# Kernel tuning notes

Measured on AMD Instinct MI355X. Metric: run time of the kernel, lower is better.

Reference implementation:

```python
import jax, jax.numpy as jnp
import numpy as np

S = 9                      # spiral length
V = [8192, 4096, 2048, 1024, 512]  # verts per level, finest -> latent


def grid_sample_bilinear(feat, grid):
    # feat [B,C,H,W], grid [B,P,2] in [-1,1]; bilinear, align_corners=True
    B, C, H, W = feat.shape
    x = (grid[..., 0] + 1.0) * 0.5 * (W - 1)
    y = (grid[..., 1] + 1.0) * 0.5 * (H - 1)
    x0 = jnp.floor(x); y0 = jnp.floor(y)
    wx = x - x0; wy = y - y0
    x0i = jnp.clip(x0.astype(jnp.int32), 0, W - 1)
    x1i = jnp.clip(x0.astype(jnp.int32) + 1, 0, W - 1)
    y0i = jnp.clip(y0.astype(jnp.int32), 0, H - 1)
    y1i = jnp.clip(y0.astype(jnp.int32) + 1, 0, H - 1)
    featf = feat.reshape(B, C, H * W).transpose(0, 2, 1)  # [B,HW,C]
    def gat(yi, xi):
        return jnp.take_along_axis(featf, (yi * W + xi)[..., None], axis=1)  # [B,P,C]
    w00 = ((1 - wy) * (1 - wx))[..., None]
    w01 = ((1 - wy) * wx)[..., None]
    w10 = (wy * (1 - wx))[..., None]
    w11 = (wy * wx)[..., None]
    return gat(y0i, x0i) * w00 + gat(y0i, x1i) * w01 + gat(y1i, x0i) * w10 + gat(y1i, x1i) * w11


def pool(x, row, col, val):
    # sparse mesh upsample: gather cols, scale, scatter-add into rows
    n_out = row.shape[0] // 3
    g = x[:, col, :] * val[None, :, None]                       # [B,nnz,C]
    return jnp.zeros((x.shape[0], n_out, x.shape[-1]), x.dtype).at[:, row, :].add(g)


def dsconv(x, idx, wd, wp, b):
    # depthwise-separable spiral conv: gather spiral ring, depthwise over S, pointwise mix
    g = x[:, idx]                                # [B,N,S,C]
    dw = jnp.einsum('bnsc,sc->bnc', g, wd)       # depthwise over spiral dim
    return jnp.einsum('bnc,co->bno', dw, wp) + b # pointwise


def _forward(uv, feat, upsample, s0, s1, s2, s3,
             row0, col0, val0, row1, col1, val1, row2, col2, val2, row3, col3, val3,
             wd0, wp0, b0, wd1, wp1, b1, wd2, wp2, b2, wd3, wp3, b3, wdh, wph, bh):
    uvc = jnp.clip((uv - 0.5) * 2.0, -1.0, 1.0)
    x = grid_sample_bilinear(feat, uvc)           # [B,P,C]  (torch: [B,C,P] then permute)
    x = jnp.einsum('vp,bpc->bvc', upsample, x)    # [B,V4,C] latent mesh features
    x = jax.nn.relu(dsconv(pool(x, row3, col3, val3), s3, wd0, wp0, b0))  # [B,1024,512]
    x = jax.nn.relu(dsconv(pool(x, row2, col2, val2), s2, wd1, wp1, b1))  # [B,2048,256]
    x = jax.nn.relu(dsconv(pool(x, row1, col1, val1), s1, wd2, wp2, b2))  # [B,4096,128]
    x = jax.nn.relu(dsconv(pool(x, row0, col0, val0), s0, wd3, wp3, b3))  # [B,8192,64]
    return dsconv(x, s0, wdh, wph, bh)            # [B,8192,3]


def setup_inputs():
    ks = jax.random.split(jax.random.key(0), 64)
    B, P, C, H, W = 8, 21, 512, 32, 32
    inp = {}
    inp['uv'] = jax.random.uniform(ks[0], (B, P, 2), jnp.float32)
    inp['feat'] = jax.random.normal(ks[1], (B, C, H, W), jnp.float32)
    inp['upsample'] = 0.01 * jnp.ones((V[4], P), jnp.float32)
    for i in range(4):
        inp[f's{i}'] = jax.random.randint(ks[2 + i], (V[i], S), 0, V[i])
    for i in range(4):
        nnz = 3 * V[i]
        inp[f'row{i}'] = jax.random.randint(ks[6 + 3 * i], (nnz,), 0, V[i])
        inp[f'col{i}'] = jax.random.randint(ks[7 + 3 * i], (nnz,), 0, V[i + 1])
        inp[f'val{i}'] = jax.random.uniform(ks[8 + 3 * i], (nnz,), jnp.float32)
    chans = [(512, 512), (512, 256), (256, 128), (128, 64), (64, 3)]
    names = ['0', '1', '2', '3', 'h']
    k = 20
    for (ci, co), nm in zip(chans, names):
        inp[f'wd{nm}'] = 0.1 * jax.random.normal(ks[k], (S, ci), jnp.float32); k += 1
        inp[f'wp{nm}'] = jax.random.normal(ks[k], (ci, co), jnp.float32) * (1.0 / float(np.sqrt(ci))); k += 1
        inp[f'b{nm}'] = jnp.zeros((co,), jnp.float32); k += 1
    return inp


def reference(uv, feat, upsample, s0, s1, s2, s3,
              row0, col0, val0, row1, col1, val1, row2, col2, val2, row3, col3, val3,
              wd0, wp0, b0, wd1, wp1, b1, wd2, wp2, b2, wd3, wp3, b3, wdh, wph, bh):
    return _forward(uv, feat, upsample, s0, s1, s2, s3,
                    row0, col0, val0, row1, col1, val1, row2, col2, val2, row3, col3, val3,
                    wd0, wp0, b0, wd1, wp1, b1, wd2, wp2, b2, wd3, wp3, b3, wdh, wph, bh)
```

## Files before the change

### kernel.cpp

```cpp
#include <hip/hip_runtime.h>

#define B_  8
#define P_  21
#define H_  32
#define W_  32

typedef float f32x4 __attribute__((ext_vector_type(4)));
typedef _Float16 f16x8 __attribute__((ext_vector_type(8)));

__device__ __forceinline__ void gload_lds16(const _Float16* g, _Float16* l) {
  __builtin_amdgcn_global_load_lds(
      (const __attribute__((address_space(1))) void*)g,
      (__attribute__((address_space(3))) void*)l, 16, 0, 0);
}

struct CsrParams {
  const int*   row[4];
  const int*   col[4];
  const float* val[4];
  int*   cnt[4];
  int*   rowptr[4];
  int*   colsout[4];
  float* valsout[4];
  int    nnz[4];
  int    V[4];
};

struct BsplitParams {
  const float* wp[4];
  int K[4], N[4], off[4];
  _Float16* b0;
  _Float16* b1;
};

__global__ __launch_bounds__(256) void k1_zero_sample(
    int* zp, int zn,
    const float* __restrict__ uv,
    const float* __restrict__ feat,
    float* __restrict__ xs) {
  int bid = blockIdx.x;
  if (bid < 60) {
    int i = bid * 256 + threadIdx.x;
    if (i < zn) zp[i] = 0;
    return;
  }
  int bp = bid - 60;
  int b  = bp / P_;
  float u0 = uv[bp * 2 + 0], u1 = uv[bp * 2 + 1];
  float gx = fminf(fmaxf((u0 - 0.5f) * 2.0f, -1.0f), 1.0f);
  float gy = fminf(fmaxf((u1 - 0.5f) * 2.0f, -1.0f), 1.0f);
  float fx = (gx + 1.0f) * 0.5f * (W_ - 1);
  float fy = (gy + 1.0f) * 0.5f * (H_ - 1);
  float x0f = floorf(fx), y0f = floorf(fy);
  float wx = fx - x0f, wy = fy - y0f;
  int x0 = (int)x0f, y0 = (int)y0f;
  int x0i = min(max(x0, 0), W_ - 1), x1i = min(max(x0 + 1, 0), W_ - 1);
  int y0i = min(max(y0, 0), H_ - 1), y1i = min(max(y0 + 1, 0), H_ - 1);
  float w00 = (1.f - wy) * (1.f - wx), w01 = (1.f - wy) * wx;
  float w10 = wy * (1.f - wx),        w11 = wy * wx;
  for (int c = threadIdx.x; c < 512; c += blockDim.x) {
    const float* fb = feat + ((size_t)(b * 512 + c)) * (H_ * W_);
    float v = fb[y0i * W_ + x0i] * w00 + fb[y0i * W_ + x1i] * w01 +
              fb[y1i * W_ + x0i] * w10 + fb[y1i * W_ + x1i] * w11;
    xs[(size_t)bp * 512 + c] = v;
  }
}

__global__ __launch_bounds__(256) void k2_count_upsample(
    CsrParams p,
    const float* __restrict__ up,
    const float* __restrict__ xs,
    float* __restrict__ xu) {
  int bid = blockIdx.x;
  if (bid < 384) {
    int l = bid / 96;
    int k = (bid - l * 96) * 256 + threadIdx.x;
    if (k < p.nnz[l]) atomicAdd(&p.cnt[l][p.row[l][k]], 1);
    return;
  }
  int b2 = bid - 384;
  int b = b2 >> 9, v = b2 & 511;
  int c2 = threadIdx.x << 1;
  float2 acc = make_float2(0.f, 0.f);
  for (int q = 0; q < P_; ++q) {
    float u = up[v * P_ + q];
    const float2 xv = *(const float2*)&xs[((size_t)(b * P_ + q)) * 512 + c2];
    acc.x = fmaf(u, xv.x, acc.x);
    acc.y = fmaf(u, xv.y, acc.y);
  }
  *(float2*)&xu[((size_t)(b * 512 + v)) * 512 + c2] = acc;
}

__global__ __launch_bounds__(256) void k3_scan_bsplit(CsrParams p, BsplitParams bp) {
  int bid = blockIdx.x;
  if (bid < 4) {
    int l = bid;
    int V = p.V[l];
    int* cnt = p.cnt[l];
    int* rp  = p.rowptr[l];
    int t = threadIdx.x;
    int chunk = V / 256;
    int base = t * chunk;
    int s = 0;
    for (int i = 0; i < chunk; ++i) s += cnt[base + i];
    __shared__ int sm[256];
    sm[t] = s;
    __syncthreads();
    for (int off = 1; off < 256; off <<= 1) {
      int v = (t >= off) ? sm[t - off] : 0;
      __syncthreads();
      sm[t] += v;
      __syncthreads();
    }
    int run = sm[t] - s;
    for (int i = 0; i < chunk; ++i) {
      int c = cnt[base + i];
      rp[base + i]  = run;
      cnt[base + i] = run;
      run += c;
    }
    if (t == 255) rp[V] = run;
    return;
  }
  int idx = (bid - 4) * 256 + threadIdx.x;
  #pragma unroll
  for (int t = 0; t < 4; ++t) {
    int sz = bp.N[t] * bp.K[t];
    if (idx < sz) {
      int K = bp.K[t];
      int n = idx / K, k = idx - n * K;
      float v = bp.wp[t][(size_t)k * bp.N[t] + n];
      _Float16 h0 = (_Float16)v;
      float r = (v - (float)h0) * 2048.0f;
      int ks = ((((k >> 3) ^ (n & 7)) << 3) | (k & 7));
      bp.b0[bp.off[t] + (size_t)n * K + ks] = h0;
      bp.b1[bp.off[t] + (size_t)n * K + ks] = (_Float16)r;
      return;
    }
    idx -= sz;
  }
}

__global__ void fill_kernel(CsrParams p) {
  int l = blockIdx.y;
  int k = blockIdx.x * 256 + threadIdx.x;
  if (k < p.nnz[l]) {
    int r = p.row[l][k];
    int pos = atomicAdd(&p.cnt[l][r], 1);
    p.colsout[l][pos] = p.col[l][k];
    p.valsout[l][pos] = p.val[l][k];
  }
}

__global__ __launch_bounds__(256) void pool_kernel(
    const float* __restrict__ x,
    const int* __restrict__ rowptr,
    const int* __restrict__ cols,
    const float* __restrict__ vals,
    float* __restrict__ out,
    int Vout, int Vin, int Cin) {
  const int lpr    = Cin >> 3;
  const int lshift = 31 - __clz(lpr);
  const int rpb    = 256 >> lshift;
  const int lr = threadIdx.x >> lshift;
  const int lc = threadIdx.x & (lpr - 1);
  const int b  = blockIdx.x & 7;
  const int n  = (blockIdx.x >> 3) * rpb + lr;
  const int c8 = lc << 3;
  const float* xb = x + (size_t)b * Vin * Cin + c8;
  int j0 = rowptr[n], j1 = rowptr[n + 1];
  int cnt = j1 - j0;
  float4 a0 = make_float4(0.f, 0.f, 0.f, 0.f);
  float4 a1 = make_float4(0.f, 0.f, 0.f, 0.f);
  if (cnt > 0) {
    int   cc[4];
    float vv[4];
    #pragma unroll
    for (int k = 0; k < 4; ++k) {
      int jj = j0 + ((k < cnt) ? k : 0);
      cc[k] = cols[jj];
      vv[k] = (k < cnt) ? vals[jj] : 0.f;
    }
    #pragma unroll
    for (int k = 0; k < 4; ++k) {
      const float* xr = xb + (size_t)cc[k] * Cin;
      float4 x0 = *(const float4*)xr;
      float4 x1 = *(const float4*)(xr + 4);
      float v = vv[k];
      a0.x = fmaf(v, x0.x, a0.x); a0.y = fmaf(v, x0.y, a0.y);
      a0.z = fmaf(v, x0.z, a0.z); a0.w = fmaf(v, x0.w, a0.w);
      a1.x = fmaf(v, x1.x, a1.x); a1.y = fmaf(v, x1.y, a1.y);
      a1.z = fmaf(v, x1.z, a1.z); a1.w = fmaf(v, x1.w, a1.w);
    }
    for (int j = j0 + 4; j < j1; ++j) {
      float v = vals[j];
      const float* xr = xb + (size_t)cols[j] * Cin;
      float4 x0 = *(const float4*)xr;
      float4 x1 = *(const float4*)(xr + 4);
      a0.x = fmaf(v, x0.x, a0.x); a0.y = fmaf(v, x0.y, a0.y);
      a0.z = fmaf(v, x0.z, a0.z); a0.w = fmaf(v, x0.w, a0.w);
      a1.x = fmaf(v, x1.x, a1.x); a1.y = fmaf(v, x1.y, a1.y);
      a1.z = fmaf(v, x1.z, a1.z); a1.w = fmaf(v, x1.w, a1.w);
    }
  }
  float* op = &out[((size_t)b * Vout + n) * Cin + c8];
  *(float4*)op = a0;
  *(float4*)(op + 4) = a1;
}

__global__ __launch_bounds__(256) void dw_split_kernel(
    const float* __restrict__ xin,
    const int* __restrict__ sidx,
    const float* __restrict__ wd,
    _Float16* __restrict__ a0o,
    _Float16* __restrict__ a1o,
    int Vout, int Cin) {
  const int lpr    = Cin >> 3;
  const int lshift = 31 - __clz(lpr);
  const int rpb    = 256 >> lshift;
  const int lr = threadIdx.x >> lshift;
  const int lc = threadIdx.x & (lpr - 1);
  const int b  = blockIdx.x & 7;
  const int n  = (blockIdx.x >> 3) * rpb + lr;
  const int c8 = lc << 3;
  const float* xb = xin + (size_t)b * Vout * Cin + c8;

  int idx[9];
  #pragma unroll
  for (int s = 0; s < 9; ++s) idx[s] = sidx[n * 9 + s];

  float4 a0 = make_float4(0.f, 0.f, 0.f, 0.f);
  float4 a1 = make_float4(0.f, 0.f, 0.f, 0.f);
  #pragma unroll
  for (int s = 0; s < 9; ++s) {
    const float* xr = xb + (size_t)idx[s] * Cin;
    float4 x0 = *(const float4*)xr;
    float4 x1 = *(const float4*)(xr + 4);
    const float* wr = wd + s * Cin + c8;
    float4 w0 = *(const float4*)wr;
    float4 w1 = *(const float4*)(wr + 4);
    a0.x = fmaf(w0.x, x0.x, a0.x); a0.y = fmaf(w0.y, x0.y, a0.y);
    a0.z = fmaf(w0.z, x0.z, a0.z); a0.w = fmaf(w0.w, x0.w, a0.w);
    a1.x = fmaf(w1.x, x1.x, a1.x); a1.y = fmaf(w1.y, x1.y, a1.y);
    a1.z = fmaf(w1.z, x1.z, a1.z); a1.w = fmaf(w1.w, x1.w, a1.w);
  }

  size_t m = (size_t)b * Vout + n;
  float v[8] = {a0.x, a0.y, a0.z, a0.w, a1.x, a1.y, a1.z, a1.w};
  f16x8 hi, lo;
  #pragma unroll
  for (int i = 0; i < 8; ++i) {
    _Float16 h0 = (_Float16)v[i];
    float r = (v[i] - (float)h0) * 2048.0f;
    hi[i] = h0;
    lo[i] = (_Float16)r;
  }
  const int c8s = (lc ^ (n & 7)) << 3;
  *(f16x8*)&a0o[m * Cin + c8s] = hi;
  *(f16x8*)&a1o[m * Cin + c8s] = lo;
}

__global__ __launch_bounds__(256) void gemm_f16x2(
    const _Float16* __restrict__ A0, const _Float16* __restrict__ A1,
    const _Float16* __restrict__ Bt0, const _Float16* __restrict__ Bt1,
    const float* __restrict__ bias, float* __restrict__ C,
    int M, int N, int K) {
  __shared__ _Float16 As[2][128 * 64];
  __shared__ _Float16 Bs[2][64 * 64];
  const int tid = threadIdx.x;
  const int bx = blockIdx.x;
  const int xr_ = (bx & 7) * (gridDim.x >> 3) + (bx >> 3);
  const int m0 = xr_ * 128, n0 = blockIdx.y * 64;
  const int wid = tid >> 6, lane = tid & 63;
  const int wr = wid >> 1, wc = wid & 1;
  const int lo = lane & 15, hi = lane >> 4;

  f32x4 accM[4][2], accC[4][2];
  #pragma unroll
  for (int mi = 0; mi < 4; ++mi)
    #pragma unroll
    for (int nj = 0; nj < 2; ++nj) {
      accM[mi][nj] = (f32x4){0.f, 0.f, 0.f, 0.f};
      accC[mi][nj] = (f32x4){0.f, 0.f, 0.f, 0.f};
    }

  const _Float16* gA[2] = {A0, A1};
  const _Float16* gB[2] = {Bt0, Bt1};

  for (int k0 = 0; k0 < K; k0 += 64) {
    #pragma unroll
    for (int p = 0; p < 2; ++p) {
      #pragma unroll
      for (int i = 0; i < 4; ++i) {
        int c = tid + 256 * i;
        int r = c >> 3, k8 = (c & 7) << 3;
        gload_lds16(gA[p] + (size_t)(m0 + r) * K + k0 + k8,
                    &As[p][(c & ~63) * 8]);
      }
      #pragma unroll
      for (int i = 0; i < 2; ++i) {
        int c = tid + 256 * i;
        int r = c >> 3, k8 = (c & 7) << 3;
        gload_lds16(gB[p] + (size_t)(n0 + r) * K + k0 + k8,
                    &Bs[p][(c & ~63) * 8]);
      }
    }
    __syncthreads();
    #pragma unroll
    for (int s = 0; s < 2; ++s) {
      const int cl = s * 4 + hi;
      f16x8 af[4][2], bf[2][2];
      #pragma unroll
      for (int mi = 0; mi < 4; ++mi) {
        const int rr = wr * 64 + mi * 16 + lo;
        const int ko = (cl ^ (rr & 7)) << 3;
        af[mi][0] = *(const f16x8*)&As[0][rr * 64 + ko];
        af[mi][1] = *(const f16x8*)&As[1][rr * 64 + ko];
      }
      #pragma unroll
      for (int nj = 0; nj < 2; ++nj) {
        const int rb = wc * 32 + nj * 16 + lo;
        const int ko = (cl ^ (rb & 7)) << 3;
        bf[nj][0] = *(const f16x8*)&Bs[0][rb * 64 + ko];
        bf[nj][1] = *(const f16x8*)&Bs[1][rb * 64 + ko];
      }
      #pragma unroll
      for (int mi = 0; mi < 4; ++mi)
        #pragma unroll
        for (int nj = 0; nj < 2; ++nj) {
          accM[mi][nj] = __builtin_amdgcn_mfma_f32_16x16x32_f16(
              af[mi][0], bf[nj][0], accM[mi][nj], 0, 0, 0);
          accC[mi][nj] = __builtin_amdgcn_mfma_f32_16x16x32_f16(
              af[mi][0], bf[nj][1], accC[mi][nj], 0, 0, 0);
          accC[mi][nj] = __builtin_amdgcn_mfma_f32_16x16x32_f16(
              af[mi][1], bf[nj][0], accC[mi][nj], 0, 0, 0);
        }
    }
    __syncthreads();
  }

  const float INV = 1.0f / 2048.0f;
  #pragma unroll
  for (int mi = 0; mi < 4; ++mi)
    #pragma unroll
    for (int nj = 0; nj < 2; ++nj) {
      int col = n0 + wc * 32 + nj * 16 + lo;
      float bv = bias[col];
      #pragma unroll
      for (int r = 0; r < 4; ++r) {
        int row = m0 + wr * 64 + mi * 16 + hi * 4 + r;
        float v = accM[mi][nj][r] + accC[mi][nj][r] * INV + bv;
        v = fmaxf(v, 0.f);
        C[(size_t)row * N + col] = v;
      }
    }
}

__global__ __launch_bounds__(256) void head_fused_kernel(
    const float* __restrict__ x,
    const int* __restrict__ sidx,
    const float* __restrict__ wdh,
    const float* __restrict__ wph,
    const float* __restrict__ bh,
    float* __restrict__ out) {
  const int bid  = blockIdx.x;
  const int b    = bid & 7;
  const int wid  = threadIdx.x >> 6;
  const int lane = threadIdx.x & 63;
  const int n    = (bid >> 3) * 4 + wid;
  const float* xb = x + (size_t)b * 8192 * 64 + lane;

  int idx[9];
  #pragma unroll
  for (int s = 0; s < 9; ++s) idx[s] = sidx[n * 9 + s];

  float acc = 0.f;
  #pragma unroll
  for (int s = 0; s < 9; ++s)
    acc = fmaf(wdh[s * 64 + lane], xb[(size_t)idx[s] * 64], acc);

  float a0 = acc * wph[lane * 3 + 0];
  float a1 = acc * wph[lane * 3 + 1];
  float a2 = acc * wph[lane * 3 + 2];
  for (int off = 32; off > 0; off >>= 1) {
    a0 += __shfl_down(a0, off);
    a1 += __shfl_down(a1, off);
    a2 += __shfl_down(a2, off);
  }
  if (lane == 0) {
    size_t row = (size_t)b * 8192 + n;
    out[row * 3 + 0] = a0 + bh[0];
    out[row * 3 + 1] = a1 + bh[1];
    out[row * 3 + 2] = a2 + bh[2];
  }
}

extern "C" void kernel_launch(void* const* d_in, const int* in_sizes, int n_in,
                              void* d_out, int out_size, void* d_ws, size_t ws_size,
                              hipStream_t stream) {
  const float* uv   = (const float*)d_in[0];
  const float* feat = (const float*)d_in[1];
  const float* up   = (const float*)d_in[2];
  const int* sArr[4] = {(const int*)d_in[3], (const int*)d_in[4],
                        (const int*)d_in[5], (const int*)d_in[6]};

  const size_t SLAB = 8ull * 2048 * 512;
  float* Wf = (float*)d_ws;
  float* S0 = Wf;
  float* S1 = Wf + SLAB;
  _Float16* A0 = (_Float16*)(S1 + SLAB);
  _Float16* A1 = A0 + SLAB;
  _Float16* Bt0all = (_Float16*)(S0 + 4500000);
  _Float16* Bt1all = Bt0all + 434176;
  float* xs = (float*)(A1 + SLAB);
  int* ib = (int*)(xs + (size_t)B_ * P_ * 512);

  int Vt[4] = {1024, 2048, 4096, 8192};
  int NZ[4] = {3072, 6144, 12288, 24576};
  int* cnt[4]; int* rp[4]; int* co[4]; float* va[4];
  {
    int* pc = ib;
    for (int t = 0; t < 4; ++t) { cnt[t] = pc; pc += Vt[t]; }
    for (int t = 0; t < 4; ++t) { rp[t] = pc; pc += Vt[t] + 1; }
    for (int t = 0; t < 4; ++t) { co[t] = pc; pc += NZ[t]; }
    float* pv = (float*)pc;
    for (int t = 0; t < 4; ++t) { va[t] = pv; pv += NZ[t]; }
  }

  CsrParams cp;
  for (int t = 0; t < 4; ++t) {
    int i = 3 - t;
    cp.row[t] = (const int*)d_in[7 + 3 * i];
    cp.col[t] = (const int*)d_in[8 + 3 * i];
    cp.val[t] = (const float*)d_in[9 + 3 * i];
    cp.cnt[t] = cnt[t]; cp.rowptr[t] = rp[t];
    cp.colsout[t] = co[t]; cp.valsout[t] = va[t];
    cp.nnz[t] = NZ[t]; cp.V[t] = Vt[t];
  }

  struct Stg { int Vin, Vout, Cin, Cout; const int* s; const float *wd, *wp, *bias; };
  Stg st[4] = {
    {512, 1024, 512, 512, sArr[3], (const float*)d_in[19], (const float*)d_in[20], (const float*)d_in[21]},
    {1024, 2048, 512, 256, sArr[2], (const float*)d_in[22], (const float*)d_in[23], (const float*)d_in[24]},
    {2048, 4096, 256, 128, sArr[1], (const float*)d_in[25], (const float*)d_in[26], (const float*)d_in[27]},
    {4096, 8192, 128, 64, sArr[0], (const float*)d_in[28], (const float*)d_in[29], (const float*)d_in[30]},
  };

  BsplitParams bp;
  int boff = 0;
  for (int t = 0; t < 4; ++t) {
    bp.wp[t] = st[t].wp;
    bp.K[t] = st[t].Cin; bp.N[t] = st[t].Cout;
    bp.off[t] = boff;
    boff += st[t].Cin * st[t].Cout;
  }
  bp.b0 = Bt0all; bp.b1 = Bt1all;
  int bsplit_blocks = (boff + 255) / 256;

  k1_zero_sample<<<60 + B_ * P_, 256, 0, stream>>>(ib, 15360, uv, feat, xs);
  k2_count_upsample<<<384 + 512 * B_, 256, 0, stream>>>(cp, up, xs, S0);
  k3_scan_bsplit<<<4 + bsplit_blocks, 256, 0, stream>>>(cp, bp);
  fill_kernel<<<dim3(96, 4), 256, 0, stream>>>(cp);

  for (int t = 0; t < 4; ++t) {
    int rpb = 2048 / st[t].Cin;
    pool_kernel<<<8 * (st[t].Vout / rpb), 256, 0, stream>>>(
        S0, rp[t], co[t], va[t], S1, st[t].Vout, st[t].Vin, st[t].Cin);
    dw_split_kernel<<<8 * (st[t].Vout / rpb), 256, 0, stream>>>(
        S1, st[t].s, st[t].wd, A0, A1, st[t].Vout, st[t].Cin);
    int M = B_ * st[t].Vout;
    gemm_f16x2<<<dim3(M / 128, st[t].Cout / 64), 256, 0, stream>>>(
        A0, A1, Bt0all + bp.off[t], Bt1all + bp.off[t],
        st[t].bias, S0, M, st[t].Cout, st[t].Cin);
  }

  head_fused_kernel<<<8 * (8192 / 4), 256, 0, stream>>>(
      S0, sArr[0], (const float*)d_in[31], (const float*)d_in[32],
      (const float*)d_in[33], (float*)d_out);
}
```

Before: 266.2 us.

## Fuse mesh pooling and spiral depthwise conv via per-block LDS staging

Each block now owns one batch and a small slice of channels across all output vertices of a level. It pools the sparse upsample into shared memory and then runs the spiral depthwise gather from LDS instead of global memory. This removes the intermediate pooled buffer round trip and one launch per level. In exchange each block loops serially over many vertices, the grid is fixed at 512 blocks, channel-slice loads are narrow and strided (2-8 floats per row), and the large LDS footprint at the finest level limits occupancy.

```diff
diff --git a/kernel.cpp b/kernel.cpp
--- a/kernel.cpp
+++ b/kernel.cpp
@@ -7,6 +7,8 @@
 
 typedef float f32x4 __attribute__((ext_vector_type(4)));
 typedef _Float16 f16x8 __attribute__((ext_vector_type(8)));
+typedef _Float16 f16x4 __attribute__((ext_vector_type(4)));
+typedef _Float16 f16x2v __attribute__((ext_vector_type(2)));
 
 __device__ __forceinline__ void gload_lds16(const _Float16* g, _Float16* l) {
   __builtin_amdgcn_global_load_lds(
@@ -152,112 +154,95 @@
   }
 }
 
-__global__ __launch_bounds__(256) void pool_kernel(
+template <int CH, int V>
+__global__ __launch_bounds__(256) void pooldw_lds_kernel(
     const float* __restrict__ x,
     const int* __restrict__ rowptr,
     const int* __restrict__ cols,
     const float* __restrict__ vals,
-    float* __restrict__ out,
-    int Vout, int Vin, int Cin) {
-  const int lpr    = Cin >> 3;
-  const int lshift = 31 - __clz(lpr);
-  const int rpb    = 256 >> lshift;
-  const int lr = threadIdx.x >> lshift;
-  const int lc = threadIdx.x & (lpr - 1);
-  const int b  = blockIdx.x & 7;
-  const int n  = (blockIdx.x >> 3) * rpb + lr;
-  const int c8 = lc << 3;
-  const float* xb = x + (size_t)b * Vin * Cin + c8;
-  int j0 = rowptr[n], j1 = rowptr[n + 1];
-  int cnt = j1 - j0;
-  float4 a0 = make_float4(0.f, 0.f, 0.f, 0.f);
-  float4 a1 = make_float4(0.f, 0.f, 0.f, 0.f);
-  if (cnt > 0) {
-    int   cc[4];
-    float vv[4];
-    #pragma unroll
-    for (int k = 0; k < 4; ++k) {
-      int jj = j0 + ((k < cnt) ? k : 0);
-      cc[k] = cols[jj];
-      vv[k] = (k < cnt) ? vals[jj] : 0.f;
-    }
-    #pragma unroll
-    for (int k = 0; k < 4; ++k) {
-      const float* xr = xb + (size_t)cc[k] * Cin;
-      float4 x0 = *(const float4*)xr;
-      float4 x1 = *(const float4*)(xr + 4);
-      float v = vv[k];
-      a0.x = fmaf(v, x0.x, a0.x); a0.y = fmaf(v, x0.y, a0.y);
-      a0.z = fmaf(v, x0.z, a0.z); a0.w = fmaf(v, x0.w, a0.w);
-      a1.x = fmaf(v, x1.x, a1.x); a1.y = fmaf(v, x1.y, a1.y);
-      a1.z = fmaf(v, x1.z, a1.z); a1.w = fmaf(v, x1.w, a1.w);
-    }
-    for (int j = j0 + 4; j < j1; ++j) {
-      float v = vals[j];
-      const float* xr = xb + (size_t)cols[j] * Cin;
-      float4 x0 = *(const float4*)xr;
-      float4 x1 = *(const float4*)(xr + 4);
-      a0.x = fmaf(v, x0.x, a0.x); a0.y = fmaf(v, x0.y, a0.y);
-      a0.z = fmaf(v, x0.z, a0.z); a0.w = fmaf(v, x0.w, a0.w);
-      a1.x = fmaf(v, x1.x, a1.x); a1.y = fmaf(v, x1.y, a1.y);
-      a1.z = fmaf(v, x1.z, a1.z); a1.w = fmaf(v, x1.w, a1.w);
-    }
-  }
-  float* op = &out[((size_t)b * Vout + n) * Cin + c8];
-  *(float4*)op = a0;
-  *(float4*)(op + 4) = a1;
-}
-
-__global__ __launch_bounds__(256) void dw_split_kernel(
-    const float* __restrict__ xin,
     const int* __restrict__ sidx,
     const float* __restrict__ wd,
     _Float16* __restrict__ a0o,
     _Float16* __restrict__ a1o,
-    int Vout, int Cin) {
-  const int lpr    = Cin >> 3;
-  const int lshift = 31 - __clz(lpr);
-  const int rpb    = 256 >> lshift;
-  const int lr = threadIdx.x >> lshift;
-  const int lc = threadIdx.x & (lpr - 1);
-  const int b  = blockIdx.x & 7;
-  const int n  = (blockIdx.x >> 3) * rpb + lr;
-  const int c8 = lc << 3;
-  const float* xb = xin + (size_t)b * Vout * Cin + c8;
-
-  int idx[9];
-  #pragma unroll
-  for (int s = 0; s < 9; ++s) idx[s] = sidx[n * 9 + s];
-
-  float4 a0 = make_float4(0.f, 0.f, 0.f, 0.f);
-  float4 a1 = make_float4(0.f, 0.f, 0.f, 0.f);
-  #pragma unroll
-  for (int s = 0; s < 9; ++s) {
-    const float* xr = xb + (size_t)idx[s] * Cin;
-    float4 x0 = *(const float4*)xr;
-    float4 x1 = *(const float4*)(xr + 4);
-    const float* wr = wd + s * Cin + c8;
-    float4 w0 = *(const float4*)wr;
-    float4 w1 = *(const float4*)(wr + 4);
-    a0.x = fmaf(w0.x, x0.x, a0.x); a0.y = fmaf(w0.y, x0.y, a0.y);
-    a0.z = fmaf(w0.z, x0.z, a0.z); a0.w = fmaf(w0.w, x0.w, a0.w);
-    a1.x = fmaf(w1.x, x1.x, a1.x); a1.y = fmaf(w1.y, x1.y, a1.y);
-    a1.z = fmaf(w1.z, x1.z, a1.z); a1.w = fmaf(w1.w, x1.w, a1.w);
-  }
-
-  size_t m = (size_t)b * Vout + n;
-  float v[8] = {a0.x, a0.y, a0.z, a0.w, a1.x, a1.y, a1.z, a1.w};
-  f16x8 hi, lo;
-  #pragma unroll
-  for (int i = 0; i < 8; ++i) {
-    _Float16 h0 = (_Float16)v[i];
-    float r = (v[i] - (float)h0) * 2048.0f;
-    hi[i] = h0;
-    lo[i] = (_Float16)r;
-  }
-  const int c8s = (lc ^ (n & 7)) << 3;
-  *(f16x8*)&a0o[m * Cin + c8s] = hi;
-  *(f16x8*)&a1o[m * Cin + c8s] = lo;
+    int Vin, int Cin) {
+  constexpr int STR = (CH == 8) ? 10 : (CH == 4 ? 7 : 3);
+  __shared__ float pooled[V * STR];
+  const int bid = blockIdx.x;
+  const int b   = bid & 7;
+  const int c0  = (bid >> 3) * CH;
+  const int t   = threadIdx.x;
+  const int R   = V >> 8;
+  const float* xb = x + (size_t)b * Vin * Cin + c0;
+
+  for (int i = 0; i < R; ++i) {
+    int n = t + (i << 8);
+    int j0 = rowptr[n], j1 = rowptr[n + 1];
+    float acc[CH];
+    #pragma unroll
+    for (int c = 0; c < CH; ++c) acc[c] = 0.f;
+    for (int j = j0; j < j1; ++j) {
+      float v = vals[j];
+      const float* xr = xb + (size_t)cols[j] * Cin;
+      if constexpr (CH == 8) {
+        float4 x0 = *(const float4*)xr;
+        float4 x1 = *(const float4*)(xr + 4);
+        acc[0] = fmaf(v, x0.x, acc[0]); acc[1] = fmaf(v, x0.y, acc[1]);
+        acc[2] = fmaf(v, x0.z, acc[2]); acc[3] = fmaf(v, x0.w, acc[3]);
+        acc[4] = fmaf(v, x1.x, acc[4]); acc[5] = fmaf(v, x1.y, acc[5]);
+        acc[6] = fmaf(v, x1.z, acc[6]); acc[7] = fmaf(v, x1.w, acc[7]);
+      } else if constexpr (CH == 4) {
+        float4 x0 = *(const float4*)xr;
+        acc[0] = fmaf(v, x0.x, acc[0]); acc[1] = fmaf(v, x0.y, acc[1]);
+        acc[2] = fmaf(v, x0.z, acc[2]); acc[3] = fmaf(v, x0.w, acc[3]);
+      } else {
+        float2 x0 = *(const float2*)xr;
+        acc[0] = fmaf(v, x0.x, acc[0]); acc[1] = fmaf(v, x0.y, acc[1]);
+      }
+    }
+    float* pr = &pooled[n * STR];
+    #pragma unroll
+    for (int c = 0; c < CH; ++c) pr[c] = acc[c];
+  }
+  __syncthreads();
+
+  for (int i = 0; i < R; ++i) {
+    int n = t + (i << 8);
+    float acc[CH];
+    #pragma unroll
+    for (int c = 0; c < CH; ++c) acc[c] = 0.f;
+    #pragma unroll
+    for (int s = 0; s < 9; ++s) {
+      int r = sidx[n * 9 + s];
+      const float* pr = &pooled[r * STR];
+      const float* wr = wd + s * Cin + c0;
+      #pragma unroll
+      for (int c = 0; c < CH; ++c)
+        acc[c] = fmaf(wr[c], pr[c], acc[c]);
+    }
+    size_t m = (size_t)b * V + n;
+    _Float16 hi[CH], lo[CH];
+    #pragma unroll
+    for (int c = 0; c < CH; ++c) {
+      _Float16 h0 = (_Float16)acc[c];
+      float rr = (acc[c] - (float)h0) * 2048.0f;
+      hi[c] = h0; lo[c] = (_Float16)rr;
+    }
+    const int cc  = c0 >> 3;
+    const int o   = c0 & 7;
+    const int pos = (((cc ^ (n & 7)) << 3) | o);
+    _Float16* p0 = &a0o[m * Cin + pos];
+    _Float16* p1 = &a1o[m * Cin + pos];
+    if constexpr (CH == 8) {
+      *(f16x8*)p0 = *(f16x8*)hi;
+      *(f16x8*)p1 = *(f16x8*)lo;
+    } else if constexpr (CH == 4) {
+      *(f16x4*)p0 = *(f16x4*)hi;
+      *(f16x4*)p1 = *(f16x4*)lo;
+    } else {
+      *(f16x2v*)p0 = *(f16x2v*)hi;
+      *(f16x2v*)p1 = *(f16x2v*)lo;
+    }
+  }
 }
 
 __global__ __launch_bounds__(256) void gemm_f16x2(
@@ -463,11 +448,19 @@
   fill_kernel<<<dim3(96, 4), 256, 0, stream>>>(cp);
 
   for (int t = 0; t < 4; ++t) {
-    int rpb = 2048 / st[t].Cin;
-    pool_kernel<<<8 * (st[t].Vout / rpb), 256, 0, stream>>>(
-        S0, rp[t], co[t], va[t], S1, st[t].Vout, st[t].Vin, st[t].Cin);
-    dw_split_kernel<<<8 * (st[t].Vout / rpb), 256, 0, stream>>>(
-        S1, st[t].s, st[t].wd, A0, A1, st[t].Vout, st[t].Cin);
+    if (t == 0)
+      pooldw_lds_kernel<8, 1024><<<512, 256, 0, stream>>>(
+          S0, rp[0], co[0], va[0], st[0].s, st[0].wd, A0, A1, st[0].Vin, st[0].Cin);
+    else if (t == 1)
+      pooldw_lds_kernel<8, 2048><<<512, 256, 0, stream>>>(
+          S0, rp[1], co[1], va[1], st[1].s, st[1].wd, A0, A1, st[1].Vin, st[1].Cin);
+    else if (t == 2)
+      pooldw_lds_kernel<4, 4096><<<512, 256, 0, stream>>>(
+          S0, rp[2], co[2], va[2], st[2].s, st[2].wd, A0, A1, st[2].Vin, st[2].Cin);
+    else
+      pooldw_lds_kernel<2, 8192><<<512, 256, 0, stream>>>(
+          S0, rp[3], co[3], va[3], st[3].s, st[3].wd, A0, A1, st[3].Vin, st[3].Cin);
+
     int M = B_ * st[t].Vout;
     gemm_f16x2<<<dim3(M / 128, st[t].Cout / 64), 256, 0, stream>>>(
         A0, A1, Bt0all + bp.off[t], Bt1all + bp.off[t],
```

Result: slower. 531.4 us (+99.6%).
